# Optimization experiments

Hardware: AMD Instinct MI355X
Metric: run time of the kernel (lower is better)

Reference implementation:

```python
import jax, jax.numpy as jnp
import numpy as np

N = 100000      # nodes
E = 400000      # edges (before self loops)
D_ATOM = 98
D_BOND = 13
EMB = 128
HEADS = 4
L = 4           # num_layer


def prelu(x, a):
    return jnp.where(x >= 0, x, a * x)


def setup_inputs() -> dict:
    key = jax.random.key(0)
    ks = jax.random.split(key, 12)
    s = 0.05
    inp = {
        "x": jax.random.normal(ks[0], (N, D_ATOM), dtype=jnp.float32),
        "edge_index": jax.random.randint(ks[1], (2, E), 0, N, dtype=jnp.int64),
        "edge_attr": jax.random.uniform(ks[2], (E, D_BOND), dtype=jnp.float32),
        # GNN-level params
        "x_emb_W": jax.random.normal(ks[3], (D_ATOM, EMB), dtype=jnp.float32) * s,
        "prelu_gnn": jnp.float32(0.25),
        # per-layer GATConv params, stacked on leading layer axis
        "wl_W": jax.random.normal(ks[4], (L, EMB, HEADS * EMB), dtype=jnp.float32) * s,
        "wl_b": jnp.zeros((L, HEADS * EMB), dtype=jnp.float32),
        "att": jax.random.normal(ks[5], (L, HEADS, 2 * EMB), dtype=jnp.float32) * s,
        "gat_bias": jnp.zeros((L, EMB), dtype=jnp.float32),
        "ee_W": jax.random.normal(ks[6], (L, D_BOND, HEADS * EMB), dtype=jnp.float32) * s,
        "ee_b": jnp.zeros((L, HEADS * EMB), dtype=jnp.float32),
        "prelu_gat": jnp.full((L,), 0.25, dtype=jnp.float32),
        # LayerNorm params per layer
        "ln_g": jnp.ones((L, EMB), dtype=jnp.float32),
        "ln_b": jnp.zeros((L, EMB), dtype=jnp.float32),
    }
    return inp


def reference(x, edge_index, edge_attr, x_emb_W, prelu_gnn, wl_W, wl_b, att,
              gat_bias, ee_W, ee_b, prelu_gat, ln_g, ln_b):
    # add self loops: (i, i) for every node; self-loop edge_attr = zeros
    loop = jnp.arange(N, dtype=edge_index.dtype)
    src = jnp.concatenate([edge_index[0], loop])  # [E+N] source (j)
    dst = jnp.concatenate([edge_index[1], loop])  # [E+N] target (i)
    ea = jnp.concatenate(
        [edge_attr, jnp.zeros((N, D_BOND), dtype=edge_attr.dtype)], axis=0)

    # input embedding + shared PReLU
    h = prelu(x @ x_emb_W, prelu_gnn)  # [N, EMB]

    for l in range(L):
        a = prelu_gat[l]
        ee = prelu(ea @ ee_W[l] + ee_b[l], a)       # [E+N, H*EMB]
        xw = prelu(h @ wl_W[l] + wl_b[l], a)        # [N, H*EMB]
        x_i = xw[dst].reshape(-1, HEADS, EMB)       # target feats
        x_j = (xw[src] + ee).reshape(-1, HEADS, EMB)  # source feats + edge emb
        # attention logits: cat([x_i,x_j]) . att
        alpha = (x_i * att[l, :, :EMB]).sum(-1) + (x_j * att[l, :, EMB:]).sum(-1)
        alpha = prelu(alpha, a)                     # [E+N, HEADS]
        # segment softmax grouped by src (edge_index[0]), as in the module
        m = jax.ops.segment_max(alpha, src, num_segments=N)
        alpha = jnp.exp(alpha - m[src])
        ssum = jax.ops.segment_sum(alpha, src, num_segments=N)
        alpha = alpha / (ssum[src] + 1e-16)
        # weighted messages, scatter-add to target nodes
        msg = (x_j * alpha[:, :, None]).reshape(-1, HEADS * EMB)
        aggr = jax.ops.segment_sum(msg, dst, num_segments=N)
        aggr = aggr.reshape(N, HEADS, EMB).mean(axis=1) + gat_bias[l]
        # LayerNorm
        mu = aggr.mean(-1, keepdims=True)
        var = ((aggr - mu) ** 2).mean(-1, keepdims=True)
        hn = (aggr - mu) / jnp.sqrt(var + 1e-5) * ln_g[l] + ln_b[l]
        # dropout is identity (drop_ratio=0); PReLU on all but last layer
        h = hn if l == L - 1 else prelu(hn, prelu_gnn)

    return h  # JK='last'
```

## Files before the change

### kernel.cpp

```cpp
#include <hip/hip_runtime.h>
#include <stdint.h>

#define NN 100000
#define NE 400000
#define NT 500000
#define DA 98
#define DB 13
#define EMB 128
#define HE 512
#define NWAVE 8192

typedef unsigned short ushort_t;
typedef __bf16 bf16x8 __attribute__((ext_vector_type(8)));
typedef float floatx4 __attribute__((ext_vector_type(4)));
typedef __fp16 fp16v2 __attribute__((ext_vector_type(2)));

__device__ __forceinline__ float prelu_f(float x, float a) { return x >= 0.f ? x : a * x; }

__device__ __forceinline__ ushort_t f2bf(float f) {
    unsigned u = __float_as_uint(f);
    unsigned r = (u + 0x7fffu + ((u >> 16) & 1u)) >> 16;
    return (ushort_t)r;
}
__device__ __forceinline__ float bflo(unsigned u) { return __uint_as_float(u << 16); }
__device__ __forceinline__ float bfhi(unsigned u) { return __uint_as_float(u & 0xffff0000u); }

__device__ __forceinline__ float dot2(unsigned a, unsigned b, float c) {
    return __builtin_amdgcn_fdot2(__builtin_bit_cast(fp16v2, a), __builtin_bit_cast(fp16v2, b), c, false);
}

__device__ __forceinline__ unsigned pk2(float lo, float hi) {
    fp16v2 p = __builtin_amdgcn_cvt_pkrtz(lo, hi);
    return __builtin_bit_cast(unsigned, p);
}

__global__ void k_count(const int* __restrict__ ei, int* __restrict__ sc, int* __restrict__ dc) {
    int e = blockIdx.x * 256 + threadIdx.x;
    if (e >= NT) return;
    int s, d;
    if (e < NE) { s = ei[e]; d = ei[NE + e]; } else { s = d = e - NE; }
    atomicAdd(sc + s, 1);
    atomicAdd(dc + d, 1);
}

__global__ void k_scan1(const int* __restrict__ cnt, int* __restrict__ part, int* __restrict__ bsum) {
    __shared__ int tmp[512];
    int t = threadIdx.x, i = blockIdx.x * 512 + t;
    int v = (i < NN) ? cnt[i] : 0;
    tmp[t] = v;
    __syncthreads();
    for (int off = 1; off < 512; off <<= 1) {
        int x = (t >= off) ? tmp[t - off] : 0;
        __syncthreads();
        tmp[t] += x;
        __syncthreads();
    }
    if (i < NN) part[i] = tmp[t] - v;
    if (t == 511) bsum[blockIdx.x] = tmp[t];
}

__global__ void k_scan2(int* __restrict__ bsum, int nb) {
    __shared__ int tmp[256];
    int t = threadIdx.x;
    int v = (t < nb) ? bsum[t] : 0;
    tmp[t] = v;
    __syncthreads();
    for (int off = 1; off < 256; off <<= 1) {
        int x = (t >= off) ? tmp[t - off] : 0;
        __syncthreads();
        tmp[t] += x;
        __syncthreads();
    }
    if (t < nb) bsum[t] = tmp[t] - v;
}

__global__ void k_scan3(const int* __restrict__ part, const int* __restrict__ bsum,
                        int* __restrict__ off, int* __restrict__ cur) {
    int i = blockIdx.x * 256 + threadIdx.x;
    if (i < NN) {
        int v = part[i] + bsum[i >> 9];
        off[i] = v;
        cur[i] = v;
    }
    if (i == 0) off[NN] = NT;
}

__global__ void k_fill(const int* __restrict__ ei, int* __restrict__ scur, int* __restrict__ dcur,
                       int* __restrict__ seid, int* __restrict__ deid) {
    int e = blockIdx.x * 256 + threadIdx.x;
    if (e >= NT) return;
    int s, d;
    if (e < NE) { s = ei[e]; d = ei[NE + e]; } else { s = d = e - NE; }
    seid[atomicAdd(scur + s, 1)] = e;
    deid[atomicAdd(dcur + d, 1)] = e;
}

__global__ void k_invperm(const int* __restrict__ seid, int* __restrict__ s2p) {
    int i = blockIdx.x * 256 + threadIdx.x;
    if (i < NT) s2p[seid[i]] = i;
}

__global__ void k_wrange(const int* __restrict__ doff, int* __restrict__ nstart) {
    int w = blockIdx.x * 256 + threadIdx.x;
    if (w > NWAVE) return;
    long long target = (long long)w * NT / NWAVE;
    int lo = 0, hi = NN;
    while (lo < hi) {
        int mid = (lo + hi) >> 1;
        if ((long long)doff[mid] < target) lo = mid + 1; else hi = mid;
    }
    nstart[w] = lo;
}

__global__ void k_dprep(const int* __restrict__ deid, const int* __restrict__ ei,
                        const float* __restrict__ ea, const int* __restrict__ s2p,
                        int* __restrict__ src_d, int* __restrict__ d2s,
                        unsigned* __restrict__ ea_d) {
    int i = blockIdx.x * 256 + threadIdx.x;
    if (i >= NT) return;
    int eid = deid[i];
    unsigned p[8] = {0, 0, 0, 0, 0, 0, 0, 0};
    int s;
    if (eid < NE) {
        s = ei[eid];
        float v[DB];
        #pragma unroll
        for (int k = 0; k < DB; ++k) v[k] = ea[(size_t)eid * DB + k];
        #pragma unroll
        for (int kp = 0; kp < 6; ++kp) p[kp] = pk2(v[2 * kp], v[2 * kp + 1]);
        p[6] = pk2(v[12], 0.f);
    } else {
        s = eid - NE;
    }
    uint4* o = (uint4*)&ea_d[(size_t)i * 8];
    o[0] = make_uint4(p[0], p[1], p[2], p[3]);
    o[1] = make_uint4(p[4], p[5], p[6], p[7]);
    src_d[i] = s;
    d2s[i] = s2p[eid];
}

__global__ void k_prep_x(const float* __restrict__ x, ushort_t* __restrict__ xb) {
    int idx = blockIdx.x * 256 + threadIdx.x;
    if (idx >= NN * 128) return;
    int col = idx & 127, n = idx >> 7;
    float v = (col < DA) ? x[(size_t)n * DA + col] : 0.f;
    xb[idx] = f2bf(v);
}

__global__ void k_prep_wx(const float* __restrict__ W, ushort_t* __restrict__ Wxt) {
    int idx = blockIdx.x * 256 + threadIdx.x;
    if (idx >= 128 * 128) return;
    int k = idx & 127, n = idx >> 7;
    float v = (k < DA) ? W[(size_t)k * EMB + n] : 0.f;
    Wxt[idx] = f2bf(v);
}

__global__ __launch_bounds__(256) void k_embed_m(const ushort_t* __restrict__ xb, const ushort_t* __restrict__ Wxt,
                                                 const float* __restrict__ pg, ushort_t* __restrict__ hb) {
    __shared__ ushort_t At[64 * 136];
    __shared__ ushort_t Bt[128 * 136];
    int t = threadIdx.x;
    int m0 = blockIdx.x * 64;
    for (int idx = t; idx < 64 * 16; idx += 256) {
        int r = idx >> 4, co = (idx & 15) * 8;
        int gr = m0 + r; if (gr >= NN) gr = 0;
        *(uint4*)&At[r * 136 + co] = *(const uint4*)&xb[(size_t)gr * 128 + co];
    }
    for (int idx = t; idx < 128 * 16; idx += 256) {
        int n = idx >> 4, ko = (idx & 15) * 8;
        *(uint4*)&Bt[n * 136 + ko] = *(const uint4*)&Wxt[n * 128 + ko];
    }
    float p = pg[0];
    __syncthreads();

    int wv = t >> 6, lane = t & 63;
    int ml = lane & 15, kq = lane >> 4;
    int n0w = wv * 32;
    floatx4 acc[4][2];
    #pragma unroll
    for (int mt = 0; mt < 4; ++mt)
        #pragma unroll
        for (int nt = 0; nt < 2; ++nt)
            acc[mt][nt] = (floatx4){0.f, 0.f, 0.f, 0.f};

    #pragma unroll
    for (int k0 = 0; k0 < 128; k0 += 32) {
        bf16x8 af[4], bfv[2];
        #pragma unroll
        for (int mt = 0; mt < 4; ++mt) {
            uint4 u = *(const uint4*)&At[(mt * 16 + ml) * 136 + k0 + kq * 8];
            af[mt] = __builtin_bit_cast(bf16x8, u);
        }
        #pragma unroll
        for (int nt = 0; nt < 2; ++nt) {
            uint4 u = *(const uint4*)&Bt[(n0w + nt * 16 + ml) * 136 + k0 + kq * 8];
            bfv[nt] = __builtin_bit_cast(bf16x8, u);
        }
        #pragma unroll
        for (int mt = 0; mt < 4; ++mt)
            #pragma unroll
            for (int nt = 0; nt < 2; ++nt)
                acc[mt][nt] = __builtin_amdgcn_mfma_f32_16x16x32_bf16(af[mt], bfv[nt], acc[mt][nt], 0, 0, 0);
    }
    #pragma unroll
    for (int nt = 0; nt < 2; ++nt) {
        int col = n0w + nt * 16 + ml;
        #pragma unroll
        for (int mt = 0; mt < 4; ++mt) {
            int row = m0 + mt * 16 + kq * 4;
            #pragma unroll
            for (int q = 0; q < 4; ++q) {
                int r = row + q;
                if (r < NN) hb[(size_t)r * EMB + col] = f2bf(prelu_f(acc[mt][nt][q], p));
            }
        }
    }
}

__global__ void k_prep(const float* __restrict__ wlW, ushort_t* __restrict__ Wtg) {
    int idx = blockIdx.x * 256 + threadIdx.x;
    if (idx >= 4 * 512 * 128) return;
    int k = idx & 127;
    int n = (idx >> 7) & 511;
    int l = idx >> 16;
    Wtg[idx] = f2bf(wlW[(size_t)l * 65536 + k * 512 + n]);
}

__global__ void k_prep_eep(const float* __restrict__ eeW, unsigned* __restrict__ eeWp) {
    int idx = blockIdx.x * 256 + threadIdx.x;
    if (idx >= 4 * 7 * 512) return;
    int l = idx / 3584;
    int rem = idx - l * 3584;
    int kp = rem >> 9;
    int ch = rem & 511;
    float lo = eeW[((size_t)l * DB + 2 * kp) * HE + ch];
    float hi = (2 * kp + 1 < DB) ? eeW[((size_t)l * DB + 2 * kp + 1) * HE + ch] : 0.f;
    eeWp[idx] = pk2(lo, hi);
}

__global__ __launch_bounds__(256) void k_gemm(const ushort_t* __restrict__ hb, const ushort_t* __restrict__ Wtg,
                                              const float* __restrict__ bl, const float* __restrict__ pa,
                                              const float* __restrict__ attl,
                                              ushort_t* __restrict__ xw,
                                              float* __restrict__ ddst, float* __restrict__ dsrc) {
    __shared__ ushort_t At[64 * 136];
    __shared__ ushort_t Bt[128 * 136];
    int t = threadIdx.x;
    int m0 = blockIdx.x * 64;
    int h = blockIdx.y;
    int n0 = h * 128;
    for (int idx = t; idx < 64 * 16; idx += 256) {
        int r = idx >> 4, co = (idx & 15) * 8;
        int gr = m0 + r; if (gr >= NN) gr = 0;
        *(uint4*)&At[r * 136 + co] = *(const uint4*)&hb[(size_t)gr * EMB + co];
    }
    for (int idx = t; idx < 128 * 16; idx += 256) {
        int n = idx >> 4, ko = (idx & 15) * 8;
        *(uint4*)&Bt[n * 136 + ko] = *(const uint4*)&Wtg[(size_t)(n0 + n) * 128 + ko];
    }
    float a = pa[0];
    __syncthreads();

    int wv = t >> 6, lane = t & 63;
    int ml = lane & 15, kq = lane >> 4;
    int n0w = wv * 32;
    floatx4 acc[4][2];
    #pragma unroll
    for (int mt = 0; mt < 4; ++mt)
        #pragma unroll
        for (int nt = 0; nt < 2; ++nt)
            acc[mt][nt] = (floatx4){0.f, 0.f, 0.f, 0.f};

    #pragma unroll
    for (int k0 = 0; k0 < 128; k0 += 32) {
        bf16x8 af[4], bfv[2];
        #pragma unroll
        for (int mt = 0; mt < 4; ++mt) {
            uint4 u = *(const uint4*)&At[(mt * 16 + ml) * 136 + k0 + kq * 8];
            af[mt] = __builtin_bit_cast(bf16x8, u);
        }
        #pragma unroll
        for (int nt = 0; nt < 2; ++nt) {
            uint4 u = *(const uint4*)&Bt[(n0w + nt * 16 + ml) * 136 + k0 + kq * 8];
            bfv[nt] = __builtin_bit_cast(bf16x8, u);
        }
        #pragma unroll
        for (int mt = 0; mt < 4; ++mt)
            #pragma unroll
            for (int nt = 0; nt < 2; ++nt)
                acc[mt][nt] = __builtin_amdgcn_mfma_f32_16x16x32_bf16(af[mt], bfv[nt], acc[mt][nt], 0, 0, 0);
    }
    __syncthreads();
    float* sdd = (float*)At;
    float* sds = (float*)At + 256;

    float pd[4][4], ps[4][4];
    #pragma unroll
    for (int mt = 0; mt < 4; ++mt)
        #pragma unroll
        for (int q = 0; q < 4; ++q) { pd[mt][q] = 0.f; ps[mt][q] = 0.f; }

    #pragma unroll
    for (int nt = 0; nt < 2; ++nt) {
        int ch = n0w + nt * 16 + ml;
        int col = n0 + ch;
        float bv = bl[col];
        float a1v = attl[h * 256 + ch];
        float a2v = attl[h * 256 + 128 + ch];
        #pragma unroll
        for (int mt = 0; mt < 4; ++mt) {
            int row = m0 + mt * 16 + kq * 4;
            #pragma unroll
            for (int q = 0; q < 4; ++q) {
                int r = row + q;
                float v = prelu_f(acc[mt][nt][q] + bv, a);
                if (r < NN) xw[(size_t)r * HE + col] = f2bf(v);
                pd[mt][q] += v * a1v;
                ps[mt][q] += v * a2v;
            }
        }
    }
    #pragma unroll
    for (int mt = 0; mt < 4; ++mt)
        #pragma unroll
        for (int q = 0; q < 4; ++q) {
            float d = pd[mt][q], s = ps[mt][q];
            #pragma unroll
            for (int m = 1; m < 16; m <<= 1) {
                d += __shfl_xor(d, m, 64);
                s += __shfl_xor(s, m, 64);
            }
            if (ml == 0) {
                int lr = mt * 16 + kq * 4 + q;
                sdd[wv * 64 + lr] = d;
                sds[wv * 64 + lr] = s;
            }
        }
    __syncthreads();
    if (t < 64) {
        int r = m0 + t;
        if (r < NN) {
            float d = sdd[t] + sdd[64 + t] + sdd[128 + t] + sdd[192 + t];
            float s = sds[t] + sds[64 + t] + sds[128 + t] + sds[192 + t];
            ddst[r * 4 + h] = d;
            dsrc[r * 4 + h] = s;
        }
    }
}

__global__ __launch_bounds__(256) void k_edge(const int* __restrict__ ei, const float* __restrict__ ea,
                                              const unsigned* __restrict__ eeWp, const float* __restrict__ ebl,
                                              const float* __restrict__ attl, const float* __restrict__ pa,
                                              const float* __restrict__ ddst, const float* __restrict__ dsrc,
                                              const int* __restrict__ s2p,
                                              float* __restrict__ alpha_s) {
    int t = threadIdx.x;
    float a = pa[0];
    int lane = t & 63;
    int wid = blockIdx.x * 4 + (t >> 6);
    int nw = gridDim.x * 4;
    int hd = lane >> 4;
    int cm = (lane & 15) * 8;
    int c0 = lane * 8;
    uint4 wpa[7], wpb[7];
    #pragma unroll
    for (int kp = 0; kp < 7; ++kp) {
        wpa[kp] = *(const uint4*)&eeWp[kp * HE + c0];
        wpb[kp] = *(const uint4*)&eeWp[kp * HE + c0 + 4];
    }
    float a2[8], eb[8];
    #pragma unroll
    for (int q = 0; q < 8; ++q) {
        a2[q] = attl[hd * 256 + 128 + cm + q];
        eb[q] = ebl[c0 + q];
    }
    float pself = 0.f;
    #pragma unroll
    for (int q = 0; q < 8; ++q) pself += prelu_f(eb[q], a) * a2[q];
    for (int e = wid; e < NT; e += nw) {
        int s, d;
        float p;
        if (e < NE) {
            s = ei[e]; d = ei[NE + e];
            float eav[DB];
            #pragma unroll
            for (int k = 0; k < DB; ++k) eav[k] = ea[(size_t)e * DB + k];
            unsigned ep[7];
            #pragma unroll
            for (int kp = 0; kp < 6; ++kp) ep[kp] = pk2(eav[2 * kp], eav[2 * kp + 1]);
            ep[6] = pk2(eav[12], 0.f);
            float v[8];
            #pragma unroll
            for (int q = 0; q < 8; ++q) v[q] = eb[q];
            #pragma unroll
            for (int kp = 0; kp < 7; ++kp) {
                v[0] = dot2(ep[kp], wpa[kp].x, v[0]);
                v[1] = dot2(ep[kp], wpa[kp].y, v[1]);
                v[2] = dot2(ep[kp], wpa[kp].z, v[2]);
                v[3] = dot2(ep[kp], wpa[kp].w, v[3]);
                v[4] = dot2(ep[kp], wpb[kp].x, v[4]);
                v[5] = dot2(ep[kp], wpb[kp].y, v[5]);
                v[6] = dot2(ep[kp], wpb[kp].z, v[6]);
                v[7] = dot2(ep[kp], wpb[kp].w, v[7]);
            }
            p = 0.f;
            #pragma unroll
            for (int q = 0; q < 8; ++q) p += prelu_f(v[q], a) * a2[q];
        } else {
            s = d = e - NE;
            p = pself;
        }
        #pragma unroll
        for (int m = 1; m < 16; m <<= 1) p += __shfl_xor(p, m, 64);
        if ((lane & 15) == 0) {
            int sp = s2p[e];
            float di = ddst[d * 4 + hd];
            float sj = dsrc[s * 4 + hd];
            alpha_s[(size_t)sp * 4 + hd] = prelu_f(di + sj + p, a);
        }
    }
}

__global__ void k_softmax(const int* __restrict__ soff, float4* __restrict__ alpha_s) {
    int n = blockIdx.x * 256 + threadIdx.x;
    if (n >= NN) return;
    int b = soff[n], e = soff[n + 1];
    float mx = -1e30f, my = -1e30f, mz = -1e30f, mw = -1e30f;
    for (int i = b; i < e; ++i) {
        float4 v = alpha_s[i];
        mx = fmaxf(mx, v.x); my = fmaxf(my, v.y);
        mz = fmaxf(mz, v.z); mw = fmaxf(mw, v.w);
    }
    float sx = 0.f, sy = 0.f, sz = 0.f, sw = 0.f;
    for (int i = b; i < e; ++i) {
        float4 v = alpha_s[i];
        v.x = __expf(v.x - mx); v.y = __expf(v.y - my);
        v.z = __expf(v.z - mz); v.w = __expf(v.w - mw);
        sx += v.x; sy += v.y; sz += v.z; sw += v.w;
        alpha_s[i] = v;
    }
    sx = 1.f / (sx + 1e-16f); sy = 1.f / (sy + 1e-16f);
    sz = 1.f / (sz + 1e-16f); sw = 1.f / (sw + 1e-16f);
    for (int i = b; i < e; ++i) {
        float4 v = alpha_s[i];
        v.x *= sx; v.y *= sy; v.z *= sz; v.w *= sw;
        alpha_s[i] = v;
    }
}

__global__ __launch_bounds__(256) void k_aggr(const int* __restrict__ nstart,
                                              const int* __restrict__ doff,
                                              const int* __restrict__ src_d, const int* __restrict__ d2s,
                                              const unsigned* __restrict__ ea_d,
                                              const unsigned* __restrict__ eeWp, const float* __restrict__ ebl,
                                              const float* __restrict__ pa, const ushort_t* __restrict__ xw,
                                              const float* __restrict__ alpha_s,
                                              const float* __restrict__ gbias, const float* __restrict__ lng,
                                              const float* __restrict__ lnb, const float* __restrict__ pgnn,
                                              int last, ushort_t* __restrict__ hb_out, float* __restrict__ fout) {
    int t = threadIdx.x;
    float a = pa[0], pg = pgnn[0];
    int lane = t & 63;
    int w = blockIdx.x * 4 + (t >> 6);
    int hd = lane >> 4;
    int cm = (lane & 15) * 8;
    int c0 = lane * 8;
    uint4 wpa[7], wpb[7];
    #pragma unroll
    for (int kp = 0; kp < 7; ++kp) {
        wpa[kp] = *(const uint4*)&eeWp[kp * HE + c0];
        wpb[kp] = *(const uint4*)&eeWp[kp * HE + c0 + 4];
    }
    float eb[8];
    #pragma unroll
    for (int q = 0; q < 8; ++q) eb[q] = ebl[c0 + q];

    int n0 = nstart[w], n1 = nstart[w + 1];
    if (n0 >= n1) return;
    int e0 = doff[n0];
    int e1 = doff[n1];
    int li = e1 - 1;

    int i1 = (e0 + 1 <= li) ? e0 + 1 : li;
    int i2 = (e0 + 2 <= li) ? e0 + 2 : li;
    int sA = src_d[e0], pA = d2s[e0];
    int sB = src_d[i1], pB = d2s[i1];
    uint4 xwA = *(const uint4*)&xw[(size_t)sA * HE + c0];
    float alA = alpha_s[(size_t)pA * 4 + hd];
    uint4 xwB = *(const uint4*)&xw[(size_t)sB * HE + c0];
    float alB = alpha_s[(size_t)pB * 4 + hd];
    int sN = src_d[i2], pN = d2s[i2];
    uint4 eaCa = *(const uint4*)&ea_d[(size_t)e0 * 8];
    uint4 eaCb = *(const uint4*)&ea_d[(size_t)e0 * 8 + 4];

    int n = n0;
    int b1 = doff[n0 + 1];
    int nn2 = (n0 + 2 <= NN) ? n0 + 2 : NN;
    int b2 = doff[nn2];
    float acc[8] = {0.f, 0.f, 0.f, 0.f, 0.f, 0.f, 0.f, 0.f};

    for (int i = e0; i < e1; ++i) {
        int ip = (i + 1 <= li) ? i + 1 : li;
        uint4 eaNa = *(const uint4*)&ea_d[(size_t)ip * 8];
        uint4 eaNb = *(const uint4*)&ea_d[(size_t)ip * 8 + 4];
        uint4 xwC = *(const uint4*)&xw[(size_t)sN * HE + c0];
        float alC = alpha_s[(size_t)pN * 4 + hd];
        int i3 = (i + 3 <= li) ? i + 3 : li;
        int sN2 = src_d[i3], pN2 = d2s[i3];
        unsigned ec[7] = {eaCa.x, eaCa.y, eaCa.z, eaCa.w, eaCb.x, eaCb.y, eaCb.z};
        float wv[8];
        #pragma unroll
        for (int q = 0; q < 8; ++q) wv[q] = eb[q];
        #pragma unroll
        for (int kp = 0; kp < 7; ++kp) {
            wv[0] = dot2(ec[kp], wpa[kp].x, wv[0]);
            wv[1] = dot2(ec[kp], wpa[kp].y, wv[1]);
            wv[2] = dot2(ec[kp], wpa[kp].z, wv[2]);
            wv[3] = dot2(ec[kp], wpa[kp].w, wv[3]);
            wv[4] = dot2(ec[kp], wpb[kp].x, wv[4]);
            wv[5] = dot2(ec[kp], wpb[kp].y, wv[5]);
            wv[6] = dot2(ec[kp], wpb[kp].z, wv[6]);
            wv[7] = dot2(ec[kp], wpb[kp].w, wv[7]);
        }
        float xv[8] = {bflo(xwA.x), bfhi(xwA.x), bflo(xwA.y), bfhi(xwA.y),
                       bflo(xwA.z), bfhi(xwA.z), bflo(xwA.w), bfhi(xwA.w)};
        #pragma unroll
        for (int q = 0; q < 8; ++q) acc[q] += (xv[q] + prelu_f(wv[q], a)) * alA;
        if (i + 1 == b1) {
            float gbv[8], gv[8], bbv[8];
            *(float4*)&gbv[0] = *(const float4*)&gbias[cm];
            *(float4*)&gbv[4] = *(const float4*)&gbias[cm + 4];
            *(float4*)&gv[0]  = *(const float4*)&lng[cm];
            *(float4*)&gv[4]  = *(const float4*)&lng[cm + 4];
            *(float4*)&bbv[0] = *(const float4*)&lnb[cm];
            *(float4*)&bbv[4] = *(const float4*)&lnb[cm + 4];
            float hm[8];
            #pragma unroll
            for (int q = 0; q < 8; ++q) {
                float v = acc[q];
                v += __shfl_xor(v, 16, 64);
                v += __shfl_xor(v, 32, 64);
                hm[q] = 0.25f * v + gbv[q];
            }
            float s8 = 0.f, q8 = 0.f;
            #pragma unroll
            for (int q = 0; q < 8; ++q) { s8 += hm[q]; q8 += hm[q] * hm[q]; }
            #pragma unroll
            for (int m = 1; m < 16; m <<= 1) {
                s8 += __shfl_xor(s8, m, 64);
                q8 += __shfl_xor(q8, m, 64);
            }
            float mu = s8 * (1.f / 128.f);
            float var = q8 * (1.f / 128.f) - mu * mu;
            float rstd = rsqrtf(var + 1e-5f);
            if (lane < 16) {
                float o[8];
                #pragma unroll
                for (int q = 0; q < 8; ++q) {
                    float v = (hm[q] - mu) * rstd * gv[q] + bbv[q];
                    o[q] = last ? v : prelu_f(v, pg);
                }
                if (last) {
                    float4* op = (float4*)&fout[(size_t)n * EMB + lane * 8];
                    op[0] = make_float4(o[0], o[1], o[2], o[3]);
                    op[1] = make_float4(o[4], o[5], o[6], o[7]);
                } else {
                    uint4 ob;
                    ob.x = (unsigned)f2bf(o[0]) | ((unsigned)f2bf(o[1]) << 16);
                    ob.y = (unsigned)f2bf(o[2]) | ((unsigned)f2bf(o[3]) << 16);
                    ob.z = (unsigned)f2bf(o[4]) | ((unsigned)f2bf(o[5]) << 16);
                    ob.w = (unsigned)f2bf(o[6]) | ((unsigned)f2bf(o[7]) << 16);
                    *(uint4*)&hb_out[(size_t)n * EMB + lane * 8] = ob;
                }
            }
            #pragma unroll
            for (int q = 0; q < 8; ++q) acc[q] = 0.f;
            ++n;
            b1 = b2;
            int nx = (n + 2 <= NN) ? n + 2 : NN;
            b2 = doff[nx];
        }
        xwA = xwB; alA = alB;
        xwB = xwC; alB = alC;
        sN = sN2; pN = pN2;
        eaCa = eaNa; eaCb = eaNb;
    }
}

extern "C" void kernel_launch(void* const* d_in, const int* in_sizes, int n_in,
                              void* d_out, int out_size, void* d_ws, size_t ws_size,
                              hipStream_t stream) {
    const float* x     = (const float*)d_in[0];
    const int*   ei    = (const int*)d_in[1];
    const float* ea    = (const float*)d_in[2];
    const float* xembW = (const float*)d_in[3];
    const float* pgnn  = (const float*)d_in[4];
    const float* wlW   = (const float*)d_in[5];
    const float* wlb   = (const float*)d_in[6];
    const float* att   = (const float*)d_in[7];
    const float* gbias = (const float*)d_in[8];
    const float* eeW   = (const float*)d_in[9];
    const float* eeb   = (const float*)d_in[10];
    const float* pgat  = (const float*)d_in[11];
    const float* lng   = (const float*)d_in[12];
    const float* lnb   = (const float*)d_in[13];

    char* w = (char*)d_ws;
    size_t off = 0;
    auto alloc = [&](size_t nbytes) -> char* {
        char* p = w + off;
        off += (nbytes + 255) & ~(size_t)255;
        return p;
    };
    ushort_t* hb    = (ushort_t*)alloc((size_t)NN * EMB * 2);
    ushort_t* xw    = (ushort_t*)alloc((size_t)NN * HE * 2);
    ushort_t* Wtg   = (ushort_t*)alloc((size_t)4 * 512 * 128 * 2);
    ushort_t* Wxt   = (ushort_t*)alloc((size_t)128 * 128 * 2);
    unsigned* eeWp  = (unsigned*)alloc((size_t)4 * 7 * 512 * 4);
    float*    ddst  = (float*)alloc((size_t)NN * 4 * 4);
    float*    dsrc  = (float*)alloc((size_t)NN * 4 * 4);
    float*    alpha = (float*)alloc((size_t)NT * 4 * 4);
    unsigned* ea_d  = (unsigned*)alloc((size_t)NT * 8 * 4);
    int* scnt   = (int*)alloc((size_t)NN * 4);
    int* dcnt   = (int*)alloc((size_t)NN * 4);
    int* soff   = (int*)alloc((size_t)(NN + 1) * 4);
    int* doff   = (int*)alloc((size_t)(NN + 1) * 4);
    int* scur   = (int*)alloc((size_t)NN * 4);
    int* dcur   = (int*)alloc((size_t)NN * 4);
    int* seid   = (int*)alloc((size_t)NT * 4);
    int* deid   = (int*)alloc((size_t)NT * 4);
    int* s2p    = (int*)alloc((size_t)NT * 4);
    int* src_d  = (int*)alloc((size_t)NT * 4);
    int* d2s    = (int*)alloc((size_t)NT * 4);
    int* nstart = (int*)alloc((size_t)(NWAVE + 1) * 4);
    int* part   = (int*)alloc((size_t)NN * 4);
    int* bsum   = (int*)alloc(256 * 4);

    ushort_t* xb = xw;

    hipMemsetAsync(scnt, 0, (size_t)NN * 4, stream);
    hipMemsetAsync(dcnt, 0, (size_t)NN * 4, stream);
    k_count<<<(NT + 255) / 256, 256, 0, stream>>>(ei, scnt, dcnt);
    k_scan1<<<196, 512, 0, stream>>>(scnt, part, bsum);
    k_scan2<<<1, 256, 0, stream>>>(bsum, 196);
    k_scan3<<<391, 256, 0, stream>>>(part, bsum, soff, scur);
    k_scan1<<<196, 512, 0, stream>>>(dcnt, part, bsum);
    k_scan2<<<1, 256, 0, stream>>>(bsum, 196);
    k_scan3<<<391, 256, 0, stream>>>(part, bsum, doff, dcur);
    k_fill<<<(NT + 255) / 256, 256, 0, stream>>>(ei, scur, dcur, seid, deid);
    k_invperm<<<(NT + 255) / 256, 256, 0, stream>>>(seid, s2p);
    k_wrange<<<(NWAVE + 1 + 255) / 256, 256, 0, stream>>>(doff, nstart);
    k_dprep<<<(NT + 255) / 256, 256, 0, stream>>>(deid, ei, ea, s2p, src_d, d2s, ea_d);
    k_prep_x<<<(NN * 128 + 255) / 256, 256, 0, stream>>>(x, xb);
    k_prep_wx<<<(128 * 128 + 255) / 256, 256, 0, stream>>>(xembW, Wxt);
    k_embed_m<<<(NN + 63) / 64, 256, 0, stream>>>(xb, Wxt, pgnn, hb);
    k_prep<<<(4 * 512 * 128 + 255) / 256, 256, 0, stream>>>(wlW, Wtg);
    k_prep_eep<<<(4 * 7 * 512 + 255) / 256, 256, 0, stream>>>(eeW, eeWp);

    for (int l = 0; l < 4; ++l) {
        const float* bl  = wlb + (size_t)l * HE;
        const float* al  = att + (size_t)l * 1024;
        const unsigned* eWl = eeWp + (size_t)l * 7 * HE;
        const float* ebl = eeb + (size_t)l * HE;
        const float* pa  = pgat + l;
        const ushort_t* Wt = Wtg + (size_t)l * 512 * 128;
        k_gemm<<<dim3((NN + 63) / 64, 4), 256, 0, stream>>>(hb, Wt, bl, pa, al, xw, ddst, dsrc);
        k_edge<<<2048, 256, 0, stream>>>(ei, ea, eWl, ebl, al, pa, ddst, dsrc, s2p, alpha);
        k_softmax<<<391, 256, 0, stream>>>(soff, (float4*)alpha);
        k_aggr<<<2048, 256, 0, stream>>>(nstart, doff, src_d, d2s, ea_d, eWl, ebl, pa, xw, alpha,
                                         gbias + (size_t)l * EMB, lng + (size_t)l * EMB,
                                         lnb + (size_t)l * EMB, pgnn, (l == 3) ? 1 : 0,
                                         hb, (float*)d_out);
    }
}
```

Measured before the change: 1.921 ms.

## Fuse edge logit computation with segment softmax over source-sorted edges

Replaces the per-edge logit kernel and the separate per-node softmax kernel with one wave-per-node-range kernel that walks edges in source-sorted order, computes logits, and normalizes each source segment in place once it completes. New precomputed source-sorted edge attributes and destination indices (plus padded arrays) let it prefetch the next edge and drop the clamped index logic in the aggregation kernel. This removes one launch per layer and the scattered writes through the source permutation. In exchange it adds a one-time prep pass and relies on wave-level shuffles and explicit waitcnt ordering for the read-after-write on alpha.

```diff
diff --git a/kernel.cpp b/kernel.cpp
--- a/kernel.cpp
+++ b/kernel.cpp
@@ -100,14 +100,14 @@
     if (i < NT) s2p[seid[i]] = i;
 }
 
-__global__ void k_wrange(const int* __restrict__ doff, int* __restrict__ nstart) {
+__global__ void k_wrange(const int* __restrict__ offs, int* __restrict__ nstart) {
     int w = blockIdx.x * 256 + threadIdx.x;
     if (w > NWAVE) return;
     long long target = (long long)w * NT / NWAVE;
     int lo = 0, hi = NN;
     while (lo < hi) {
         int mid = (lo + hi) >> 1;
-        if ((long long)doff[mid] < target) lo = mid + 1; else hi = mid;
+        if ((long long)offs[mid] < target) lo = mid + 1; else hi = mid;
     }
     nstart[w] = lo;
 }
@@ -117,26 +117,56 @@
                         int* __restrict__ src_d, int* __restrict__ d2s,
                         unsigned* __restrict__ ea_d) {
     int i = blockIdx.x * 256 + threadIdx.x;
-    if (i >= NT) return;
-    int eid = deid[i];
+    if (i >= NT + 4) return;
     unsigned p[8] = {0, 0, 0, 0, 0, 0, 0, 0};
-    int s;
-    if (eid < NE) {
-        s = ei[eid];
-        float v[DB];
-        #pragma unroll
-        for (int k = 0; k < DB; ++k) v[k] = ea[(size_t)eid * DB + k];
-        #pragma unroll
-        for (int kp = 0; kp < 6; ++kp) p[kp] = pk2(v[2 * kp], v[2 * kp + 1]);
-        p[6] = pk2(v[12], 0.f);
-    } else {
-        s = eid - NE;
+    int s = 0, pos = 0;
+    if (i < NT) {
+        int eid = deid[i];
+        if (eid < NE) {
+            s = ei[eid];
+            float v[DB];
+            #pragma unroll
+            for (int k = 0; k < DB; ++k) v[k] = ea[(size_t)eid * DB + k];
+            #pragma unroll
+            for (int kp = 0; kp < 6; ++kp) p[kp] = pk2(v[2 * kp], v[2 * kp + 1]);
+            p[6] = pk2(v[12], 0.f);
+        } else {
+            s = eid - NE;
+        }
+        pos = s2p[eid];
     }
     uint4* o = (uint4*)&ea_d[(size_t)i * 8];
     o[0] = make_uint4(p[0], p[1], p[2], p[3]);
     o[1] = make_uint4(p[4], p[5], p[6], p[7]);
     src_d[i] = s;
-    d2s[i] = s2p[eid];
+    d2s[i] = pos;
+}
+
+__global__ void k_sprep(const int* __restrict__ seid, const int* __restrict__ ei,
+                        const float* __restrict__ ea,
+                        int* __restrict__ dst_s, unsigned* __restrict__ ea_s) {
+    int i = blockIdx.x * 256 + threadIdx.x;
+    if (i >= NT + 4) return;
+    unsigned p[8] = {0, 0, 0, 0, 0, 0, 0, 0};
+    int d = 0;
+    if (i < NT) {
+        int eid = seid[i];
+        if (eid < NE) {
+            d = ei[NE + eid];
+            float v[DB];
+            #pragma unroll
+            for (int k = 0; k < DB; ++k) v[k] = ea[(size_t)eid * DB + k];
+            #pragma unroll
+            for (int kp = 0; kp < 6; ++kp) p[kp] = pk2(v[2 * kp], v[2 * kp + 1]);
+            p[6] = pk2(v[12], 0.f);
+        } else {
+            d = eid - NE;
+        }
+    }
+    uint4* o = (uint4*)&ea_s[(size_t)i * 8];
+    o[0] = make_uint4(p[0], p[1], p[2], p[3]);
+    o[1] = make_uint4(p[4], p[5], p[6], p[7]);
+    dst_s[i] = d;
 }
 
 __global__ void k_prep_x(const float* __restrict__ x, ushort_t* __restrict__ xb) {
@@ -348,17 +378,18 @@
     }
 }
 
-__global__ __launch_bounds__(256) void k_edge(const int* __restrict__ ei, const float* __restrict__ ea,
-                                              const unsigned* __restrict__ eeWp, const float* __restrict__ ebl,
-                                              const float* __restrict__ attl, const float* __restrict__ pa,
-                                              const float* __restrict__ ddst, const float* __restrict__ dsrc,
-                                              const int* __restrict__ s2p,
-                                              float* __restrict__ alpha_s) {
+__global__ __launch_bounds__(256) void k_edgesm(const int* __restrict__ nstart_s,
+                                                const int* __restrict__ soff,
+                                                const unsigned* __restrict__ ea_s,
+                                                const int* __restrict__ dst_s,
+                                                const unsigned* __restrict__ eeWp, const float* __restrict__ ebl,
+                                                const float* __restrict__ attl, const float* __restrict__ pa,
+                                                const float* __restrict__ ddst, const float* __restrict__ dsrc,
+                                                float* __restrict__ alpha_s) {
     int t = threadIdx.x;
     float a = pa[0];
     int lane = t & 63;
-    int wid = blockIdx.x * 4 + (t >> 6);
-    int nw = gridDim.x * 4;
+    int w = blockIdx.x * 4 + (t >> 6);
     int hd = lane >> 4;
     int cm = (lane & 15) * 8;
     int c0 = lane * 8;
@@ -374,77 +405,95 @@
         a2[q] = attl[hd * 256 + 128 + cm + q];
         eb[q] = ebl[c0 + q];
     }
-    float pself = 0.f;
-    #pragma unroll
-    for (int q = 0; q < 8; ++q) pself += prelu_f(eb[q], a) * a2[q];
-    for (int e = wid; e < NT; e += nw) {
-        int s, d;
-        float p;
-        if (e < NE) {
-            s = ei[e]; d = ei[NE + e];
-            float eav[DB];
-            #pragma unroll
-            for (int k = 0; k < DB; ++k) eav[k] = ea[(size_t)e * DB + k];
-            unsigned ep[7];
-            #pragma unroll
-            for (int kp = 0; kp < 6; ++kp) ep[kp] = pk2(eav[2 * kp], eav[2 * kp + 1]);
-            ep[6] = pk2(eav[12], 0.f);
-            float v[8];
-            #pragma unroll
-            for (int q = 0; q < 8; ++q) v[q] = eb[q];
-            #pragma unroll
-            for (int kp = 0; kp < 7; ++kp) {
-                v[0] = dot2(ep[kp], wpa[kp].x, v[0]);
-                v[1] = dot2(ep[kp], wpa[kp].y, v[1]);
-                v[2] = dot2(ep[kp], wpa[kp].z, v[2]);
-                v[3] = dot2(ep[kp], wpa[kp].w, v[3]);
-                v[4] = dot2(ep[kp], wpb[kp].x, v[4]);
-                v[5] = dot2(ep[kp], wpb[kp].y, v[5]);
-                v[6] = dot2(ep[kp], wpb[kp].z, v[6]);
-                v[7] = dot2(ep[kp], wpb[kp].w, v[7]);
-            }
-            p = 0.f;
-            #pragma unroll
-            for (int q = 0; q < 8; ++q) p += prelu_f(v[q], a) * a2[q];
-        } else {
-            s = d = e - NE;
-            p = pself;
-        }
+    int head = lane & 3;
+
+    int n0 = nstart_s[w], n1 = nstart_s[w + 1];
+    if (n0 >= n1) return;
+    int e0 = soff[n0], e1 = soff[n1];
+
+    uint4 eaAa = *(const uint4*)&ea_s[(size_t)e0 * 8];
+    uint4 eaAb = *(const uint4*)&ea_s[(size_t)e0 * 8 + 4];
+    int dA = dst_s[e0], dB = dst_s[e0 + 1];
+    float diA = ddst[dA * 4 + hd];
+
+    int n = n0;
+    int b = e0;
+    int bEnd = soff[n0 + 1];
+    float sj = dsrc[n * 4 + hd];
+    float mx = -1e30f;
+
+    for (int i = e0; i < e1; ++i) {
+        uint4 eaNa = *(const uint4*)&ea_s[(size_t)(i + 1) * 8];
+        uint4 eaNb = *(const uint4*)&ea_s[(size_t)(i + 1) * 8 + 4];
+        int dC = dst_s[i + 2];
+        float diB = ddst[dB * 4 + hd];
+        unsigned ec[7] = {eaAa.x, eaAa.y, eaAa.z, eaAa.w, eaAb.x, eaAb.y, eaAb.z};
+        float v[8];
+        #pragma unroll
+        for (int q = 0; q < 8; ++q) v[q] = eb[q];
+        #pragma unroll
+        for (int kp = 0; kp < 7; ++kp) {
+            v[0] = dot2(ec[kp], wpa[kp].x, v[0]);
+            v[1] = dot2(ec[kp], wpa[kp].y, v[1]);
+            v[2] = dot2(ec[kp], wpa[kp].z, v[2]);
+            v[3] = dot2(ec[kp], wpa[kp].w, v[3]);
+            v[4] = dot2(ec[kp], wpb[kp].x, v[4]);
+            v[5] = dot2(ec[kp], wpb[kp].y, v[5]);
+            v[6] = dot2(ec[kp], wpb[kp].z, v[6]);
+            v[7] = dot2(ec[kp], wpb[kp].w, v[7]);
+        }
+        float p = 0.f;
+        #pragma unroll
+        for (int q = 0; q < 8; ++q) p += prelu_f(v[q], a) * a2[q];
         #pragma unroll
         for (int m = 1; m < 16; m <<= 1) p += __shfl_xor(p, m, 64);
         if ((lane & 15) == 0) {
-            int sp = s2p[e];
-            float di = ddst[d * 4 + hd];
-            float sj = dsrc[s * 4 + hd];
-            alpha_s[(size_t)sp * 4 + hd] = prelu_f(di + sj + p, a);
-        }
-    }
-}
-
-__global__ void k_softmax(const int* __restrict__ soff, float4* __restrict__ alpha_s) {
-    int n = blockIdx.x * 256 + threadIdx.x;
-    if (n >= NN) return;
-    int b = soff[n], e = soff[n + 1];
-    float mx = -1e30f, my = -1e30f, mz = -1e30f, mw = -1e30f;
-    for (int i = b; i < e; ++i) {
-        float4 v = alpha_s[i];
-        mx = fmaxf(mx, v.x); my = fmaxf(my, v.y);
-        mz = fmaxf(mz, v.z); mw = fmaxf(mw, v.w);
-    }
-    float sx = 0.f, sy = 0.f, sz = 0.f, sw = 0.f;
-    for (int i = b; i < e; ++i) {
-        float4 v = alpha_s[i];
-        v.x = __expf(v.x - mx); v.y = __expf(v.y - my);
-        v.z = __expf(v.z - mz); v.w = __expf(v.w - mw);
-        sx += v.x; sy += v.y; sz += v.z; sw += v.w;
-        alpha_s[i] = v;
-    }
-    sx = 1.f / (sx + 1e-16f); sy = 1.f / (sy + 1e-16f);
-    sz = 1.f / (sz + 1e-16f); sw = 1.f / (sw + 1e-16f);
-    for (int i = b; i < e; ++i) {
-        float4 v = alpha_s[i];
-        v.x *= sx; v.y *= sy; v.z *= sz; v.w *= sw;
-        alpha_s[i] = v;
+            float lg = prelu_f(diA + sj + p, a);
+            alpha_s[(size_t)i * 4 + hd] = lg;
+            mx = fmaxf(mx, lg);
+        }
+        if (i + 1 == bEnd) {
+            float m0v = __shfl(mx, 0, 64), m1v = __shfl(mx, 16, 64),
+                  m2v = __shfl(mx, 32, 64), m3v = __shfl(mx, 48, 64);
+            float mh = head == 0 ? m0v : head == 1 ? m1v : head == 2 ? m2v : m3v;
+            asm volatile("s_waitcnt vmcnt(0)" ::: "memory");
+            int deg = bEnd - b;
+            if (deg <= 16) {
+                int idx = b + (lane >> 2);
+                bool act = idx < bEnd;
+                float x = act ? alpha_s[(size_t)idx * 4 + head] : 0.f;
+                float ex = act ? __expf(x - mh) : 0.f;
+                float s = ex;
+                #pragma unroll
+                for (int m = 4; m < 64; m <<= 1) s += __shfl_xor(s, m, 64);
+                float inv = 1.f / (s + 1e-16f);
+                if (act) alpha_s[(size_t)idx * 4 + head] = ex * inv;
+            } else {
+                float s = 0.f;
+                for (int idx = b + (lane >> 2); idx < bEnd; idx += 16) {
+                    float x = alpha_s[(size_t)idx * 4 + head];
+                    float ex = __expf(x - mh);
+                    s += ex;
+                    alpha_s[(size_t)idx * 4 + head] = ex;
+                }
+                #pragma unroll
+                for (int m = 4; m < 64; m <<= 1) s += __shfl_xor(s, m, 64);
+                float inv = 1.f / (s + 1e-16f);
+                asm volatile("s_waitcnt vmcnt(0)" ::: "memory");
+                for (int idx = b + (lane >> 2); idx < bEnd; idx += 16)
+                    alpha_s[(size_t)idx * 4 + head] *= inv;
+            }
+            ++n;
+            if (i + 1 < e1) {
+                b = bEnd;
+                bEnd = soff[n + 1];
+                sj = dsrc[n * 4 + hd];
+                mx = -1e30f;
+            }
+        }
+        eaAa = eaNa; eaAb = eaNb;
+        dA = dB; dB = dC;
+        diA = diB;
     }
 }
 
@@ -479,17 +528,14 @@
     if (n0 >= n1) return;
     int e0 = doff[n0];
     int e1 = doff[n1];
-    int li = e1 - 1;
-
-    int i1 = (e0 + 1 <= li) ? e0 + 1 : li;
-    int i2 = (e0 + 2 <= li) ? e0 + 2 : li;
+
     int sA = src_d[e0], pA = d2s[e0];
-    int sB = src_d[i1], pB = d2s[i1];
+    int sB = src_d[e0 + 1], pB = d2s[e0 + 1];
     uint4 xwA = *(const uint4*)&xw[(size_t)sA * HE + c0];
     float alA = alpha_s[(size_t)pA * 4 + hd];
     uint4 xwB = *(const uint4*)&xw[(size_t)sB * HE + c0];
     float alB = alpha_s[(size_t)pB * 4 + hd];
-    int sN = src_d[i2], pN = d2s[i2];
+    int sN = src_d[e0 + 2], pN = d2s[e0 + 2];
     uint4 eaCa = *(const uint4*)&ea_d[(size_t)e0 * 8];
     uint4 eaCb = *(const uint4*)&ea_d[(size_t)e0 * 8 + 4];
 
@@ -500,13 +546,11 @@
     float acc[8] = {0.f, 0.f, 0.f, 0.f, 0.f, 0.f, 0.f, 0.f};
 
     for (int i = e0; i < e1; ++i) {
-        int ip = (i + 1 <= li) ? i + 1 : li;
-        uint4 eaNa = *(const uint4*)&ea_d[(size_t)ip * 8];
-        uint4 eaNb = *(const uint4*)&ea_d[(size_t)ip * 8 + 4];
+        uint4 eaNa = *(const uint4*)&ea_d[(size_t)(i + 1) * 8];
+        uint4 eaNb = *(const uint4*)&ea_d[(size_t)(i + 1) * 8 + 4];
         uint4 xwC = *(const uint4*)&xw[(size_t)sN * HE + c0];
         float alC = alpha_s[(size_t)pN * 4 + hd];
-        int i3 = (i + 3 <= li) ? i + 3 : li;
-        int sN2 = src_d[i3], pN2 = d2s[i3];
+        int sN2 = src_d[i + 3], pN2 = d2s[i + 3];
         unsigned ec[7] = {eaCa.x, eaCa.y, eaCa.z, eaCa.w, eaCb.x, eaCb.y, eaCb.z};
         float wv[8];
         #pragma unroll
@@ -620,21 +664,24 @@
     float*    ddst  = (float*)alloc((size_t)NN * 4 * 4);
     float*    dsrc  = (float*)alloc((size_t)NN * 4 * 4);
     float*    alpha = (float*)alloc((size_t)NT * 4 * 4);
-    unsigned* ea_d  = (unsigned*)alloc((size_t)NT * 8 * 4);
-    int* scnt   = (int*)alloc((size_t)NN * 4);
-    int* dcnt   = (int*)alloc((size_t)NN * 4);
-    int* soff   = (int*)alloc((size_t)(NN + 1) * 4);
-    int* doff   = (int*)alloc((size_t)(NN + 1) * 4);
-    int* scur   = (int*)alloc((size_t)NN * 4);
-    int* dcur   = (int*)alloc((size_t)NN * 4);
-    int* seid   = (int*)alloc((size_t)NT * 4);
-    int* deid   = (int*)alloc((size_t)NT * 4);
-    int* s2p    = (int*)alloc((size_t)NT * 4);
-    int* src_d  = (int*)alloc((size_t)NT * 4);
-    int* d2s    = (int*)alloc((size_t)NT * 4);
-    int* nstart = (int*)alloc((size_t)(NWAVE + 1) * 4);
-    int* part   = (int*)alloc((size_t)NN * 4);
-    int* bsum   = (int*)alloc(256 * 4);
+    unsigned* ea_d  = (unsigned*)alloc((size_t)(NT + 4) * 8 * 4);
+    unsigned* ea_s  = (unsigned*)alloc((size_t)(NT + 4) * 8 * 4);
+    int* scnt     = (int*)alloc((size_t)NN * 4);
+    int* dcnt     = (int*)alloc((size_t)NN * 4);
+    int* soff     = (int*)alloc((size_t)(NN + 1) * 4);
+    int* doff     = (int*)alloc((size_t)(NN + 1) * 4);
+    int* scur     = (int*)alloc((size_t)NN * 4);
+    int* dcur     = (int*)alloc((size_t)NN * 4);
+    int* seid     = (int*)alloc((size_t)NT * 4);
+    int* deid     = (int*)alloc((size_t)NT * 4);
+    int* s2p      = (int*)alloc((size_t)NT * 4);
+    int* src_d    = (int*)alloc((size_t)(NT + 4) * 4);
+    int* d2s      = (int*)alloc((size_t)(NT + 4) * 4);
+    int* dst_s    = (int*)alloc((size_t)(NT + 4) * 4);
+    int* nstart   = (int*)alloc((size_t)(NWAVE + 1) * 4);
+    int* nstart_s = (int*)alloc((size_t)(NWAVE + 1) * 4);
+    int* part     = (int*)alloc((size_t)NN * 4);
+    int* bsum     = (int*)alloc(256 * 4);
 
     ushort_t* xb = xw;
 
@@ -650,7 +697,9 @@
     k_fill<<<(NT + 255) / 256, 256, 0, stream>>>(ei, scur, dcur, seid, deid);
     k_invperm<<<(NT + 255) / 256, 256, 0, stream>>>(seid, s2p);
     k_wrange<<<(NWAVE + 1 + 255) / 256, 256, 0, stream>>>(doff, nstart);
-    k_dprep<<<(NT + 255) / 256, 256, 0, stream>>>(deid, ei, ea, s2p, src_d, d2s, ea_d);
+    k_wrange<<<(NWAVE + 1 + 255) / 256, 256, 0, stream>>>(soff, nstart_s);
+    k_dprep<<<(NT + 4 + 255) / 256, 256, 0, stream>>>(deid, ei, ea, s2p, src_d, d2s, ea_d);
+    k_sprep<<<(NT + 4 + 255) / 256, 256, 0, stream>>>(seid, ei, ea, dst_s, ea_s);
     k_prep_x<<<(NN * 128 + 255) / 256, 256, 0, stream>>>(x, xb);
     k_prep_wx<<<(128 * 128 + 255) / 256, 256, 0, stream>>>(xembW, Wxt);
     k_embed_m<<<(NN + 63) / 64, 256, 0, stream>>>(xb, Wxt, pgnn, hb);
@@ -665,8 +714,8 @@
         const float* pa  = pgat + l;
         const ushort_t* Wt = Wtg + (size_t)l * 512 * 128;
         k_gemm<<<dim3((NN + 63) / 64, 4), 256, 0, stream>>>(hb, Wt, bl, pa, al, xw, ddst, dsrc);
-        k_edge<<<2048, 256, 0, stream>>>(ei, ea, eWl, ebl, al, pa, ddst, dsrc, s2p, alpha);
-        k_softmax<<<391, 256, 0, stream>>>(soff, (float4*)alpha);
+        k_edgesm<<<2048, 256, 0, stream>>>(nstart_s, soff, ea_s, dst_s, eWl, ebl, al, pa,
+                                           ddst, dsrc, alpha);
         k_aggr<<<2048, 256, 0, stream>>>(nstart, doff, src_d, d2s, ea_d, eWl, ebl, pa, xw, alpha,
                                          gbias + (size_t)l * EMB, lng + (size_t)l * EMB,
                                          lnb + (size_t)l * EMB, pgnn, (l == 3) ? 1 : 0,
```

Result: faster. 1.832 ms (-4.6%).
